# Performance work log

Measured on AMD Instinct MI355X. Metric: run time of the kernel, lower is better.

The kernel has to match this reference:

```python
import jax, jax.numpy as jnp
import numpy as np

N_NODES = 50000
N_EDGES = 600000
IN_DIM = 128
HIDDEN = 256
OUT_DIM = 16


def setup_inputs() -> dict:
    key = jax.random.key(0)
    ks = jax.random.split(key, 10)
    x = jax.random.normal(ks[0], (N_NODES, IN_DIM), dtype=jnp.float32)
    edge_index = jax.random.randint(ks[1], (2, N_EDGES), 0, N_NODES, dtype=jnp.int64)
    s = 0.05
    return {
        "x": x,
        "edge_index": edge_index,
        # conv1 MLP: Linear(IN_DIM->HIDDEN), Linear(HIDDEN->HIDDEN)
        "w1a": jax.random.normal(ks[2], (IN_DIM, HIDDEN), dtype=jnp.float32) * s,
        "b1a": jnp.zeros((HIDDEN,), dtype=jnp.float32),
        "w2a": jax.random.normal(ks[3], (HIDDEN, HIDDEN), dtype=jnp.float32) * s,
        "b2a": jnp.zeros((HIDDEN,), dtype=jnp.float32),
        # conv2 MLP: Linear(HIDDEN->HIDDEN), Linear(HIDDEN->OUT_DIM)
        "w1b": jax.random.normal(ks[4], (HIDDEN, HIDDEN), dtype=jnp.float32) * s,
        "b1b": jnp.zeros((HIDDEN,), dtype=jnp.float32),
        "w2b": jax.random.normal(ks[5], (HIDDEN, OUT_DIM), dtype=jnp.float32) * s,
        "b2b": jnp.zeros((OUT_DIM,), dtype=jnp.float32),
    }


def _gin_conv(h, src, dst, w1, b1, w2, b2):
    # GINConv with eps=0: MLP(h_i + sum_{j: (j->i)} h_j)
    agg = jax.ops.segment_sum(h[src], dst, num_segments=N_NODES)  # [N, D]
    z = h + agg
    z = jax.nn.relu(z @ w1 + b1)
    return z @ w2 + b2


def reference(x, edge_index, w1a, b1a, w2a, b2a, w1b, b1b, w2b, b2b):
    src, dst = edge_index[0], edge_index[1]
    h = _gin_conv(x, src, dst, w1a, b1a, w2a, b2a)
    h = jax.nn.relu(h)  # dropout p=0.0 -> identity
    h = _gin_conv(h, src, dst, w1b, b1b, w2b, b2b)
    return jax.nn.log_softmax(h, axis=1)
```

## Files before the change

### kernel.cpp

```cpp
#include <hip/hip_runtime.h>

#define NN 50000
#define NE 600000
#define SCAN_BLOCKS 196

typedef short v8s __attribute__((ext_vector_type(8)));
typedef float v4f __attribute__((ext_vector_type(4)));

#define LAW 72
#define MTW 264

__device__ __forceinline__ float b2f(ushort u) {
    union { unsigned u; float f; } v; v.u = ((unsigned)u) << 16; return v.f;
}
__device__ __forceinline__ float uaf(unsigned u) {
    union { unsigned u; float f; } v; v.u = u; return v.f;
}
__device__ __forceinline__ ushort f2b(float f) {
    union { float f; unsigned u; } v; v.f = f;
    unsigned r = v.u + 0x7FFFu + ((v.u >> 16) & 1u);
    return (ushort)(r >> 16);
}

__global__ __launch_bounds__(256) void detect_idx_kernel(const int* __restrict__ raw,
                                                          int* __restrict__ flag) {
    __shared__ int cnt;
    if (threadIdx.x == 0) cnt = 0;
    __syncthreads();
    int c = 0;
    for (int i = threadIdx.x; i < 2048; i += 256)
        if (raw[2 * i + 1] != 0) c++;
    atomicAdd(&cnt, c);
    __syncthreads();
    if (threadIdx.x == 0) *flag = (cnt > 10) ? 1 : 0;
}

__global__ __launch_bounds__(256) void convert_idx_kernel(const void* __restrict__ raw,
                                                           const int* __restrict__ flag,
                                                           int* __restrict__ out,
                                                           int* __restrict__ deg, int n) {
    int i = blockIdx.x * 256 + threadIdx.x;
    if (i >= n) return;
    int v;
    if (*flag) v = ((const int*)raw)[i];
    else       v = (int)((const long long*)raw)[i];
    out[i] = v;
    if (i >= NE) atomicAdd(&deg[v], 1);
}

__global__ __launch_bounds__(256) void block_sum_kernel(const int* __restrict__ deg,
                                                         int* __restrict__ bsum) {
    const int i = blockIdx.x * 256 + threadIdx.x;
    int v = (i < NN) ? deg[i] : 0;
#pragma unroll
    for (int o = 32; o; o >>= 1) v += __shfl_down(v, o, 64);
    __shared__ int ws[4];
    if ((threadIdx.x & 63) == 0) ws[threadIdx.x >> 6] = v;
    __syncthreads();
    if (threadIdx.x == 0) bsum[blockIdx.x] = ws[0] + ws[1] + ws[2] + ws[3];
}

__global__ __launch_bounds__(256) void scan_sums_kernel(const int* __restrict__ bsum,
                                                         int* __restrict__ boff,
                                                         int* __restrict__ rowptr) {
    __shared__ int tmp[256];
    const int t = threadIdx.x;
    const int v = (t < SCAN_BLOCKS) ? bsum[t] : 0;
    tmp[t] = v;
    __syncthreads();
#pragma unroll
    for (int off = 1; off < 256; off <<= 1) {
        int u = (t >= off) ? tmp[t - off] : 0;
        __syncthreads();
        tmp[t] += u;
        __syncthreads();
    }
    boff[t] = tmp[t] - v;
    if (t == 255) rowptr[NN] = tmp[255];
}

__global__ __launch_bounds__(256) void block_scan_kernel(const int* __restrict__ deg,
                                                          const int* __restrict__ boff,
                                                          int* __restrict__ rowptr,
                                                          int* __restrict__ cursor) {
    const int t = threadIdx.x;
    const int i = blockIdx.x * 256 + t;
    const int lane = t & 63, w = t >> 6;
    const int v = (i < NN) ? deg[i] : 0;
    int s = v;
#pragma unroll
    for (int o = 1; o < 64; o <<= 1) {
        int u = __shfl_up(s, o, 64);
        if (lane >= o) s += u;
    }
    __shared__ int wsum[4];
    if (lane == 63) wsum[w] = s;
    __syncthreads();
    int wpre = 0;
    for (int k = 0; k < w; k++) wpre += wsum[k];
    const int excl = boff[blockIdx.x] + wpre + s - v;
    if (i < NN) {
        rowptr[i] = excl;
        cursor[i] = excl;
    }
}

__global__ __launch_bounds__(256) void fill_csr_kernel(const int* __restrict__ srcIdx,
                                                        const int* __restrict__ dstIdx,
                                                        int* __restrict__ cursor,
                                                        int* __restrict__ csr_src) {
    int e = blockIdx.x * 256 + threadIdx.x;
    if (e >= NE) return;
    int pos = atomicAdd(&cursor[dstIdx[e]], 1);
    csr_src[pos] = srcIdx[e];
}

__global__ __launch_bounds__(256) void cvt_f32_bf16_kernel(const float* __restrict__ in,
                                                            ushort* __restrict__ out, int n4) {
    int i = blockIdx.x * 256 + threadIdx.x;
    if (i >= n4) return;
    const float4 v = *(const float4*)&in[(size_t)i * 4];
    ushort4 o;
    o.x = f2b(v.x); o.y = f2b(v.y); o.z = f2b(v.z); o.w = f2b(v.w);
    *(ushort4*)&out[(size_t)i * 4] = o;
}

__global__ __launch_bounds__(256) void pack_w1_kernel(const float* __restrict__ in,
                                                       ushort* __restrict__ out, int K1) {
    int o = blockIdx.x * 256 + threadIdx.x;
    if (o >= K1 * 256) return;
    int j = o & 7, lane = (o >> 3) & 63, f = o >> 9;
    int kk = f & 1, n = (f >> 1) & 3, wv = (f >> 3) & 3, s = f >> 5;
    int k = s * 64 + kk * 32 + (lane >> 4) * 8 + j;
    int col = wv * 64 + n * 16 + (lane & 15);
    out[o] = f2b(in[(size_t)k * 256 + col]);
}

__global__ __launch_bounds__(256) void pack_w2_kernel(const float* __restrict__ in,
                                                       ushort* __restrict__ out) {
    int o = blockIdx.x * 256 + threadIdx.x;
    if (o >= 256 * 256) return;
    int j = o & 7, lane = (o >> 3) & 63, f = o >> 9;
    int kk = f & 3, n = (f >> 2) & 3, wv = (f >> 4) & 3, kh = f >> 6;
    int k = kh * 128 + kk * 32 + (lane >> 4) * 8 + j;
    int col = wv * 64 + n * 16 + (lane & 15);
    out[o] = f2b(in[(size_t)k * 256 + col]);
}

__global__ __launch_bounds__(256) void pack_wh_kernel(const float* __restrict__ in,
                                                       ushort* __restrict__ out) {
    int o = blockIdx.x * 256 + threadIdx.x;
    if (o >= 4096) return;
    int j = o & 7, lane = (o >> 3) & 63, k8 = o >> 9;
    int k = k8 * 32 + (lane >> 4) * 8 + j;
    int col = lane & 15;
    out[o] = f2b(in[(size_t)k * 16 + col]);
}

template <int D>
__global__ __launch_bounds__(256) void aggregate_bf16_kernel(const ushort* __restrict__ feat,
                                                              ushort* __restrict__ z,
                                                              const int* __restrict__ rowptr,
                                                              const int* __restrict__ csr_src) {
    const int node = __builtin_amdgcn_readfirstlane(blockIdx.x * 4 + (threadIdx.x >> 6));
    const int lane = threadIdx.x & 63;
    if (node >= NN) return;
    const int rbeg = rowptr[node];
    const int rend = rowptr[node + 1];

    if constexpr (D == 256) {
        const size_t base = (size_t)node * 256 + lane * 4;
        const uint2 sv = *(const uint2*)&feat[base];
        float a0 = uaf(sv.x << 16), a1 = uaf(sv.x & 0xFFFF0000u);
        float a2 = uaf(sv.y << 16), a3 = uaf(sv.y & 0xFFFF0000u);
        int j = rbeg;
        for (; j + 7 < rend; j += 8) {
            uint2 v[8];
#pragma unroll
            for (int q = 0; q < 8; q++)
                v[q] = *(const uint2*)&feat[(size_t)csr_src[j + q] * 256 + lane * 4];
#pragma unroll
            for (int q = 0; q < 8; q++) {
                a0 += uaf(v[q].x << 16); a1 += uaf(v[q].x & 0xFFFF0000u);
                a2 += uaf(v[q].y << 16); a3 += uaf(v[q].y & 0xFFFF0000u);
            }
        }
        for (; j + 3 < rend; j += 4) {
            uint2 v[4];
#pragma unroll
            for (int q = 0; q < 4; q++)
                v[q] = *(const uint2*)&feat[(size_t)csr_src[j + q] * 256 + lane * 4];
#pragma unroll
            for (int q = 0; q < 4; q++) {
                a0 += uaf(v[q].x << 16); a1 += uaf(v[q].x & 0xFFFF0000u);
                a2 += uaf(v[q].y << 16); a3 += uaf(v[q].y & 0xFFFF0000u);
            }
        }
        for (; j < rend; j++) {
            const uint2 v = *(const uint2*)&feat[(size_t)csr_src[j] * 256 + lane * 4];
            a0 += uaf(v.x << 16); a1 += uaf(v.x & 0xFFFF0000u);
            a2 += uaf(v.y << 16); a3 += uaf(v.y & 0xFFFF0000u);
        }
        uint2 o;
        o.x = (uint)f2b(a0) | ((uint)f2b(a1) << 16);
        o.y = (uint)f2b(a2) | ((uint)f2b(a3) << 16);
        *(uint2*)&z[base] = o;
    } else {
        const size_t base = (size_t)node * 128 + lane * 2;
        const uint sv = *(const uint*)&feat[base];
        float a0 = uaf(sv << 16), a1 = uaf(sv & 0xFFFF0000u);
        int j = rbeg;
        for (; j + 7 < rend; j += 8) {
            uint v[8];
#pragma unroll
            for (int q = 0; q < 8; q++)
                v[q] = *(const uint*)&feat[(size_t)csr_src[j + q] * 128 + lane * 2];
#pragma unroll
            for (int q = 0; q < 8; q++) {
                a0 += uaf(v[q] << 16); a1 += uaf(v[q] & 0xFFFF0000u);
            }
        }
        for (; j + 3 < rend; j += 4) {
            uint v[4];
#pragma unroll
            for (int q = 0; q < 4; q++)
                v[q] = *(const uint*)&feat[(size_t)csr_src[j + q] * 128 + lane * 2];
#pragma unroll
            for (int q = 0; q < 4; q++) {
                a0 += uaf(v[q] << 16); a1 += uaf(v[q] & 0xFFFF0000u);
            }
        }
        for (; j < rend; j++) {
            const uint v = *(const uint*)&feat[(size_t)csr_src[j] * 128 + lane * 2];
            a0 += uaf(v << 16); a1 += uaf(v & 0xFFFF0000u);
        }
        *(uint*)&z[base] = (uint)f2b(a0) | ((uint)f2b(a1) << 16);
    }
}

template <int K1, bool HEAD>
__global__ __launch_bounds__(256) void fused_mlp_kernel(const ushort* __restrict__ A,
                                                         const ushort* __restrict__ W1p,
                                                         const float* __restrict__ b1,
                                                         const ushort* __restrict__ W2p,
                                                         const float* __restrict__ b2,
                                                         void* __restrict__ outp, int M) {
    constexpr int S = K1 / 64;
    __shared__ ushort lA[2][64 * LAW];
    __shared__ ushort mT[64 * MTW];
    const int tid = threadIdx.x;
    const int lane = tid & 63;
    const int wv = tid >> 6;
    const int row0 = blockIdx.x * 64;
    const int l15 = lane & 15;
    const int kq = lane >> 4;
    const int ar = tid >> 2, ak = (tid & 3) * 16;

    const bool aok = (row0 + ar) < M;
    const ushort* Arow = A + (size_t)(row0 + ar) * K1 + ak;

    v4f acc[4][4];
#pragma unroll
    for (int m = 0; m < 4; m++)
#pragma unroll
        for (int n = 0; n < 4; n++) acc[m][n] = (v4f){0.f, 0.f, 0.f, 0.f};

    v8s a0 = {}, a1v = {};
    v8s w1cur[4][2], w1nxt[4][2];

    if (aok) { a0 = *(const v8s*)Arow; a1v = *(const v8s*)(Arow + 8); }
#pragma unroll
    for (int n = 0; n < 4; n++)
#pragma unroll
        for (int kk = 0; kk < 2; kk++)
            w1cur[n][kk] = *(const v8s*)(W1p + (size_t)(wv * 8 + n * 2 + kk) * 512 + lane * 8);
    *(v8s*)&lA[0][ar * LAW + ak]     = a0;
    *(v8s*)&lA[0][ar * LAW + ak + 8] = a1v;

#pragma unroll
    for (int s = 0; s < S; s++) {
        __syncthreads();
        if (s + 1 < S) {
            a0 = (v8s){}; a1v = (v8s){};
            if (aok) {
                a0  = *(const v8s*)(Arow + (s + 1) * 64);
                a1v = *(const v8s*)(Arow + (s + 1) * 64 + 8);
            }
#pragma unroll
            for (int n = 0; n < 4; n++)
#pragma unroll
                for (int kk = 0; kk < 2; kk++)
                    w1nxt[n][kk] = *(const v8s*)(W1p + (size_t)((s + 1) * 32 + wv * 8 + n * 2 + kk) * 512 + lane * 8);
        }
        v8s af[4][2];
#pragma unroll
        for (int m = 0; m < 4; m++)
#pragma unroll
            for (int kk = 0; kk < 2; kk++)
                af[m][kk] = *(const v8s*)&lA[s & 1][(m * 16 + l15) * LAW + kk * 32 + kq * 8];
#pragma unroll
        for (int kk = 0; kk < 2; kk++)
#pragma unroll
            for (int m = 0; m < 4; m++)
#pragma unroll
                for (int n = 0; n < 4; n++)
                    acc[m][n] = __builtin_amdgcn_mfma_f32_16x16x32_bf16(af[m][kk], w1cur[n][kk], acc[m][n], 0, 0, 0);
        if (s + 1 < S) {
            *(v8s*)&lA[(s + 1) & 1][ar * LAW + ak]     = a0;
            *(v8s*)&lA[(s + 1) & 1][ar * LAW + ak + 8] = a1v;
#pragma unroll
            for (int n = 0; n < 4; n++)
#pragma unroll
                for (int kk = 0; kk < 2; kk++)
                    w1cur[n][kk] = w1nxt[n][kk];
        }
    }

#pragma unroll
    for (int n = 0; n < 4; n++) {
        const int gc = wv * 64 + n * 16 + l15;
        const float bv = b1[gc];
#pragma unroll
        for (int m = 0; m < 4; m++)
#pragma unroll
            for (int r = 0; r < 4; r++)
                mT[(m * 16 + kq * 4 + r) * MTW + gc] = f2b(fmaxf(acc[m][n][r] + bv, 0.f));
    }
    __syncthreads();

    if constexpr (!HEAD) {
#pragma unroll
        for (int m = 0; m < 4; m++)
#pragma unroll
            for (int n = 0; n < 4; n++) acc[m][n] = (v4f){0.f, 0.f, 0.f, 0.f};
#pragma unroll
        for (int kh = 0; kh < 2; kh++) {
            v8s w2r[4][4];
#pragma unroll
            for (int n = 0; n < 4; n++)
#pragma unroll
                for (int kk = 0; kk < 4; kk++)
                    w2r[n][kk] = *(const v8s*)(W2p + (size_t)(kh * 64 + wv * 16 + n * 4 + kk) * 512 + lane * 8);
#pragma unroll
            for (int kk = 0; kk < 4; kk++) {
                v8s a2[4];
#pragma unroll
                for (int m = 0; m < 4; m++)
                    a2[m] = *(const v8s*)&mT[(m * 16 + l15) * MTW + kh * 128 + kk * 32 + kq * 8];
#pragma unroll
                for (int m = 0; m < 4; m++)
#pragma unroll
                    for (int n = 0; n < 4; n++)
                        acc[m][n] = __builtin_amdgcn_mfma_f32_16x16x32_bf16(a2[m], w2r[n][kk], acc[m][n], 0, 0, 0);
            }
        }
        __syncthreads();
#pragma unroll
        for (int n = 0; n < 4; n++) {
            const int gc = wv * 64 + n * 16 + l15;
            const float bv = b2[gc];
#pragma unroll
            for (int m = 0; m < 4; m++)
#pragma unroll
                for (int r = 0; r < 4; r++)
                    mT[(m * 16 + kq * 4 + r) * MTW + gc] = f2b(fmaxf(acc[m][n][r] + bv, 0.f));
        }
        __syncthreads();
        ushort* C = (ushort*)outp;
        const int brow = tid >> 5, bcol = (tid & 31) * 8;
#pragma unroll
        for (int i = 0; i < 8; i++) {
            const int row = i * 8 + brow;
            if (row0 + row < M) {
                const v8s v = *(const v8s*)&mT[row * MTW + bcol];
                *(v8s*)&C[(size_t)(row0 + row) * 256 + bcol] = v;
            }
        }
    } else {
        v4f h = (v4f){0.f, 0.f, 0.f, 0.f};
        v8s w2r[8];
#pragma unroll
        for (int k8 = 0; k8 < 8; k8++)
            w2r[k8] = *(const v8s*)(W2p + (size_t)k8 * 512 + lane * 8);
#pragma unroll
        for (int k8 = 0; k8 < 8; k8++) {
            const v8s a2 = *(const v8s*)&mT[(wv * 16 + l15) * MTW + k8 * 32 + kq * 8];
            h = __builtin_amdgcn_mfma_f32_16x16x32_bf16(a2, w2r[k8], h, 0, 0, 0);
        }
        float* O = (float*)outp;
        const float bv = b2[l15];
#pragma unroll
        for (int r = 0; r < 4; r++) {
            const float v = h[r] + bv;
            float mx = v;
#pragma unroll
            for (int o = 8; o; o >>= 1) mx = fmaxf(mx, __shfl_xor(mx, o, 16));
            const float e = expf(v - mx);
            float sl = e;
#pragma unroll
            for (int o = 8; o; o >>= 1) sl += __shfl_xor(sl, o, 16);
            const int grow = row0 + wv * 16 + kq * 4 + r;
            if (grow < M) O[(size_t)grow * 16 + l15] = (v - mx) - logf(sl);
        }
    }
}

extern "C" void kernel_launch(void* const* d_in, const int* in_sizes, int n_in,
                              void* d_out, int out_size, void* d_ws, size_t ws_size,
                              hipStream_t stream) {
    (void)in_sizes; (void)n_in; (void)out_size; (void)ws_size;
    const float* x   = (const float*)d_in[0];
    const void*  ei  = d_in[1];
    const float* w1a = (const float*)d_in[2];
    const float* b1a = (const float*)d_in[3];
    const float* w2a = (const float*)d_in[4];
    const float* b2a = (const float*)d_in[5];
    const float* w1b = (const float*)d_in[6];
    const float* b1b = (const float*)d_in[7];
    const float* w2b = (const float*)d_in[8];
    const float* b2b = (const float*)d_in[9];
    float* out = (float*)d_out;

    ushort* XB   = (ushort*)d_ws;
    ushort* Z1   = XB + (size_t)NN * 128;
    ushort* H1   = Z1 + (size_t)NN * 128;
    ushort* Z2   = H1 + (size_t)NN * 256;
    ushort* W1pa = Z2 + (size_t)NN * 256;
    ushort* W2pa = W1pa + 128 * 256;
    ushort* W1pb = W2pa + 256 * 256;
    ushort* W2hp = W1pb + 256 * 256;
    int* idx     = (int*)(W2hp + 16 * 256);
    int* flag    = idx + 2 * NE;
    int* deg     = flag + 1;
    int* rowptr  = deg + NN;
    int* cursor  = rowptr + NN + 1;
    int* csr_src = cursor + NN;
    int* bsum    = csr_src + NE;
    int* boff    = bsum + SCAN_BLOCKS;

    detect_idx_kernel<<<1, 256, 0, stream>>>((const int*)ei, flag);
    hipMemsetAsync(deg, 0, NN * sizeof(int), stream);
    convert_idx_kernel<<<(2 * NE + 255) / 256, 256, 0, stream>>>(ei, flag, idx, deg, 2 * NE);
    const int* srcI = idx;
    const int* dstI = idx + NE;
    block_sum_kernel<<<SCAN_BLOCKS, 256, 0, stream>>>(deg, bsum);
    scan_sums_kernel<<<1, 256, 0, stream>>>(bsum, boff, rowptr);
    block_scan_kernel<<<SCAN_BLOCKS, 256, 0, stream>>>(deg, boff, rowptr, cursor);
    fill_csr_kernel<<<(NE + 255) / 256, 256, 0, stream>>>(srcI, dstI, cursor, csr_src);

    cvt_f32_bf16_kernel<<<(NN * 128 / 4 + 255) / 256, 256, 0, stream>>>(x, XB, NN * 128 / 4);
    pack_w1_kernel<<<(128 * 256 + 255) / 256, 256, 0, stream>>>(w1a, W1pa, 128);
    pack_w2_kernel<<<(256 * 256 + 255) / 256, 256, 0, stream>>>(w2a, W2pa);
    pack_w1_kernel<<<(256 * 256 + 255) / 256, 256, 0, stream>>>(w1b, W1pb, 256);
    pack_wh_kernel<<<(4096 + 255) / 256, 256, 0, stream>>>(w2b, W2hp);

    const int aggBlocks = (NN + 3) / 4;
    const int mlpBlocks = (NN + 63) / 64;

    aggregate_bf16_kernel<128><<<aggBlocks, 256, 0, stream>>>(XB, Z1, rowptr, csr_src);
    fused_mlp_kernel<128, false><<<mlpBlocks, 256, 0, stream>>>(Z1, W1pa, b1a, W2pa, b2a, H1, NN);

    aggregate_bf16_kernel<256><<<aggBlocks, 256, 0, stream>>>(H1, Z2, rowptr, csr_src);
    fused_mlp_kernel<256, true><<<mlpBlocks, 256, 0, stream>>>(Z2, W1pb, b1b, W2hp, b2b, out, NN);
}
```

Before: 201.8 us.

## Fuse neighbor aggregation into MLP kernel and read raw edge indices directly

The separate aggregation kernels are folded into the MLP kernel. Each block gathers and sums neighbor features for its 64 rows straight into shared memory, then runs the MFMA GEMMs from there, so the Z1/Z2 intermediates never round-trip through global memory. The edge-index conversion pass is dropped: degree counting and CSR fill read the raw int32 or int64 indices directly, and the four weight-packing launches are merged into one. In exchange the gather now runs at fewer waves per node block, with larger shared memory and no double-buffered A prefetch, which may lower occupancy and latency hiding during the gather.

```diff
diff --git a/kernel.cpp b/kernel.cpp
--- a/kernel.cpp
+++ b/kernel.cpp
@@ -7,12 +7,8 @@
 typedef short v8s __attribute__((ext_vector_type(8)));
 typedef float v4f __attribute__((ext_vector_type(4)));
 
-#define LAW 72
 #define MTW 264
 
-__device__ __forceinline__ float b2f(ushort u) {
-    union { unsigned u; float f; } v; v.u = ((unsigned)u) << 16; return v.f;
-}
 __device__ __forceinline__ float uaf(unsigned u) {
     union { unsigned u; float f; } v; v.u = u; return v.f;
 }
@@ -35,17 +31,15 @@
     if (threadIdx.x == 0) *flag = (cnt > 10) ? 1 : 0;
 }
 
-__global__ __launch_bounds__(256) void convert_idx_kernel(const void* __restrict__ raw,
-                                                           const int* __restrict__ flag,
-                                                           int* __restrict__ out,
-                                                           int* __restrict__ deg, int n) {
-    int i = blockIdx.x * 256 + threadIdx.x;
-    if (i >= n) return;
-    int v;
-    if (*flag) v = ((const int*)raw)[i];
-    else       v = (int)((const long long*)raw)[i];
-    out[i] = v;
-    if (i >= NE) atomicAdd(&deg[v], 1);
+__global__ __launch_bounds__(256) void count_deg_raw_kernel(const void* __restrict__ raw,
+                                                             const int* __restrict__ flag,
+                                                             int* __restrict__ deg) {
+    int e = blockIdx.x * 256 + threadIdx.x;
+    if (e >= NE) return;
+    int d;
+    if (*flag) d = ((const int*)raw)[NE + e];
+    else       d = (int)((const long long*)raw)[NE + e];
+    atomicAdd(&deg[d], 1);
 }
 
 __global__ __launch_bounds__(256) void block_sum_kernel(const int* __restrict__ deg,
@@ -105,14 +99,22 @@
     }
 }
 
-__global__ __launch_bounds__(256) void fill_csr_kernel(const int* __restrict__ srcIdx,
-                                                        const int* __restrict__ dstIdx,
-                                                        int* __restrict__ cursor,
-                                                        int* __restrict__ csr_src) {
+__global__ __launch_bounds__(256) void fill_csr_raw_kernel(const void* __restrict__ raw,
+                                                            const int* __restrict__ flag,
+                                                            int* __restrict__ cursor,
+                                                            int* __restrict__ csr_src) {
     int e = blockIdx.x * 256 + threadIdx.x;
     if (e >= NE) return;
-    int pos = atomicAdd(&cursor[dstIdx[e]], 1);
-    csr_src[pos] = srcIdx[e];
+    int s, d;
+    if (*flag) {
+        s = ((const int*)raw)[e];
+        d = ((const int*)raw)[NE + e];
+    } else {
+        s = (int)((const long long*)raw)[e];
+        d = (int)((const long long*)raw)[NE + e];
+    }
+    int pos = atomicAdd(&cursor[d], 1);
+    csr_src[pos] = s;
 }
 
 __global__ __launch_bounds__(256) void cvt_f32_bf16_kernel(const float* __restrict__ in,
@@ -125,128 +127,54 @@
     *(ushort4*)&out[(size_t)i * 4] = o;
 }
 
-__global__ __launch_bounds__(256) void pack_w1_kernel(const float* __restrict__ in,
-                                                       ushort* __restrict__ out, int K1) {
-    int o = blockIdx.x * 256 + threadIdx.x;
-    if (o >= K1 * 256) return;
+__device__ __forceinline__ void pack_w1_elem(const float* in, ushort* out, int o, int K1) {
     int j = o & 7, lane = (o >> 3) & 63, f = o >> 9;
     int kk = f & 1, n = (f >> 1) & 3, wv = (f >> 3) & 3, s = f >> 5;
     int k = s * 64 + kk * 32 + (lane >> 4) * 8 + j;
     int col = wv * 64 + n * 16 + (lane & 15);
     out[o] = f2b(in[(size_t)k * 256 + col]);
 }
-
-__global__ __launch_bounds__(256) void pack_w2_kernel(const float* __restrict__ in,
-                                                       ushort* __restrict__ out) {
-    int o = blockIdx.x * 256 + threadIdx.x;
-    if (o >= 256 * 256) return;
-    int j = o & 7, lane = (o >> 3) & 63, f = o >> 9;
-    int kk = f & 3, n = (f >> 2) & 3, wv = (f >> 4) & 3, kh = f >> 6;
-    int k = kh * 128 + kk * 32 + (lane >> 4) * 8 + j;
-    int col = wv * 64 + n * 16 + (lane & 15);
-    out[o] = f2b(in[(size_t)k * 256 + col]);
-}
-
-__global__ __launch_bounds__(256) void pack_wh_kernel(const float* __restrict__ in,
-                                                       ushort* __restrict__ out) {
-    int o = blockIdx.x * 256 + threadIdx.x;
-    if (o >= 4096) return;
-    int j = o & 7, lane = (o >> 3) & 63, k8 = o >> 9;
-    int k = k8 * 32 + (lane >> 4) * 8 + j;
-    int col = lane & 15;
-    out[o] = f2b(in[(size_t)k * 16 + col]);
-}
-
-template <int D>
-__global__ __launch_bounds__(256) void aggregate_bf16_kernel(const ushort* __restrict__ feat,
-                                                              ushort* __restrict__ z,
-                                                              const int* __restrict__ rowptr,
-                                                              const int* __restrict__ csr_src) {
-    const int node = __builtin_amdgcn_readfirstlane(blockIdx.x * 4 + (threadIdx.x >> 6));
-    const int lane = threadIdx.x & 63;
-    if (node >= NN) return;
-    const int rbeg = rowptr[node];
-    const int rend = rowptr[node + 1];
-
-    if constexpr (D == 256) {
-        const size_t base = (size_t)node * 256 + lane * 4;
-        const uint2 sv = *(const uint2*)&feat[base];
-        float a0 = uaf(sv.x << 16), a1 = uaf(sv.x & 0xFFFF0000u);
-        float a2 = uaf(sv.y << 16), a3 = uaf(sv.y & 0xFFFF0000u);
-        int j = rbeg;
-        for (; j + 7 < rend; j += 8) {
-            uint2 v[8];
-#pragma unroll
-            for (int q = 0; q < 8; q++)
-                v[q] = *(const uint2*)&feat[(size_t)csr_src[j + q] * 256 + lane * 4];
-#pragma unroll
-            for (int q = 0; q < 8; q++) {
-                a0 += uaf(v[q].x << 16); a1 += uaf(v[q].x & 0xFFFF0000u);
-                a2 += uaf(v[q].y << 16); a3 += uaf(v[q].y & 0xFFFF0000u);
-            }
-        }
-        for (; j + 3 < rend; j += 4) {
-            uint2 v[4];
-#pragma unroll
-            for (int q = 0; q < 4; q++)
-                v[q] = *(const uint2*)&feat[(size_t)csr_src[j + q] * 256 + lane * 4];
-#pragma unroll
-            for (int q = 0; q < 4; q++) {
-                a0 += uaf(v[q].x << 16); a1 += uaf(v[q].x & 0xFFFF0000u);
-                a2 += uaf(v[q].y << 16); a3 += uaf(v[q].y & 0xFFFF0000u);
-            }
-        }
-        for (; j < rend; j++) {
-            const uint2 v = *(const uint2*)&feat[(size_t)csr_src[j] * 256 + lane * 4];
-            a0 += uaf(v.x << 16); a1 += uaf(v.x & 0xFFFF0000u);
-            a2 += uaf(v.y << 16); a3 += uaf(v.y & 0xFFFF0000u);
-        }
-        uint2 o;
-        o.x = (uint)f2b(a0) | ((uint)f2b(a1) << 16);
-        o.y = (uint)f2b(a2) | ((uint)f2b(a3) << 16);
-        *(uint2*)&z[base] = o;
+__global__ __launch_bounds__(256) void pack_all_kernel(const float* __restrict__ w1a,
+                                                        const float* __restrict__ w2a,
+                                                        const float* __restrict__ w1b,
+                                                        const float* __restrict__ wh,
+                                                        ushort* __restrict__ W1pa,
+                                                        ushort* __restrict__ W2pa,
+                                                        ushort* __restrict__ W1pb,
+                                                        ushort* __restrict__ W2hp) {
+    const int b = blockIdx.x;
+    if (b < 128) {
+        pack_w1_elem(w1a, W1pa, b * 256 + threadIdx.x, 128);
+    } else if (b < 384) {
+        int o = (b - 128) * 256 + threadIdx.x;
+        int j = o & 7, lane = (o >> 3) & 63, f = o >> 9;
+        int kk = f & 3, n = (f >> 2) & 3, wv = (f >> 4) & 3, kh = f >> 6;
+        int k = kh * 128 + kk * 32 + (lane >> 4) * 8 + j;
+        int col = wv * 64 + n * 16 + (lane & 15);
+        W2pa[o] = f2b(w2a[(size_t)k * 256 + col]);
+    } else if (b < 640) {
+        pack_w1_elem(w1b, W1pb, (b - 384) * 256 + threadIdx.x, 256);
     } else {
-        const size_t base = (size_t)node * 128 + lane * 2;
-        const uint sv = *(const uint*)&feat[base];
-        float a0 = uaf(sv << 16), a1 = uaf(sv & 0xFFFF0000u);
-        int j = rbeg;
-        for (; j + 7 < rend; j += 8) {
-            uint v[8];
-#pragma unroll
-            for (int q = 0; q < 8; q++)
-                v[q] = *(const uint*)&feat[(size_t)csr_src[j + q] * 128 + lane * 2];
-#pragma unroll
-            for (int q = 0; q < 8; q++) {
-                a0 += uaf(v[q] << 16); a1 += uaf(v[q] & 0xFFFF0000u);
-            }
-        }
-        for (; j + 3 < rend; j += 4) {
-            uint v[4];
-#pragma unroll
-            for (int q = 0; q < 4; q++)
-                v[q] = *(const uint*)&feat[(size_t)csr_src[j + q] * 128 + lane * 2];
-#pragma unroll
-            for (int q = 0; q < 4; q++) {
-                a0 += uaf(v[q] << 16); a1 += uaf(v[q] & 0xFFFF0000u);
-            }
-        }
-        for (; j < rend; j++) {
-            const uint v = *(const uint*)&feat[(size_t)csr_src[j] * 128 + lane * 2];
-            a0 += uaf(v << 16); a1 += uaf(v & 0xFFFF0000u);
-        }
-        *(uint*)&z[base] = (uint)f2b(a0) | ((uint)f2b(a1) << 16);
+        int o = (b - 640) * 256 + threadIdx.x;
+        int j = o & 7, lane = (o >> 3) & 63, k8 = o >> 9;
+        int k = k8 * 32 + (lane >> 4) * 8 + j;
+        int col = lane & 15;
+        W2hp[o] = f2b(wh[(size_t)k * 16 + col]);
     }
 }
 
 template <int K1, bool HEAD>
-__global__ __launch_bounds__(256) void fused_mlp_kernel(const ushort* __restrict__ A,
+__global__ __launch_bounds__(256) void fused_gin_kernel(const ushort* __restrict__ feat,
+                                                         const int* __restrict__ rowptr,
+                                                         const int* __restrict__ csr_src,
                                                          const ushort* __restrict__ W1p,
                                                          const float* __restrict__ b1,
                                                          const ushort* __restrict__ W2p,
                                                          const float* __restrict__ b2,
                                                          void* __restrict__ outp, int M) {
     constexpr int S = K1 / 64;
-    __shared__ ushort lA[2][64 * LAW];
+    constexpr int ZW = K1 + 8;
+    __shared__ ushort zT[64 * ZW];
     __shared__ ushort mT[64 * MTW];
     const int tid = threadIdx.x;
     const int lane = tid & 63;
@@ -254,66 +182,113 @@
     const int row0 = blockIdx.x * 64;
     const int l15 = lane & 15;
     const int kq = lane >> 4;
-    const int ar = tid >> 2, ak = (tid & 3) * 16;
-
-    const bool aok = (row0 + ar) < M;
-    const ushort* Arow = A + (size_t)(row0 + ar) * K1 + ak;
+
+    for (int t = 0; t < 16; t++) {
+        const int r = wv * 16 + t;
+        const int node = __builtin_amdgcn_readfirstlane(row0 + r);
+        ushort* zrow = &zT[r * ZW];
+        if (node < M) {
+            const int rbeg = rowptr[node];
+            const int rend = rowptr[node + 1];
+            if constexpr (K1 == 256) {
+                const uint2 sv = *(const uint2*)&feat[(size_t)node * 256 + lane * 4];
+                float a0 = uaf(sv.x << 16), a1 = uaf(sv.x & 0xFFFF0000u);
+                float a2 = uaf(sv.y << 16), a3 = uaf(sv.y & 0xFFFF0000u);
+                int j = rbeg;
+                for (; j + 7 < rend; j += 8) {
+                    uint2 v[8];
+#pragma unroll
+                    for (int q = 0; q < 8; q++)
+                        v[q] = *(const uint2*)&feat[(size_t)csr_src[j + q] * 256 + lane * 4];
+#pragma unroll
+                    for (int q = 0; q < 8; q++) {
+                        a0 += uaf(v[q].x << 16); a1 += uaf(v[q].x & 0xFFFF0000u);
+                        a2 += uaf(v[q].y << 16); a3 += uaf(v[q].y & 0xFFFF0000u);
+                    }
+                }
+                for (; j + 3 < rend; j += 4) {
+                    uint2 v[4];
+#pragma unroll
+                    for (int q = 0; q < 4; q++)
+                        v[q] = *(const uint2*)&feat[(size_t)csr_src[j + q] * 256 + lane * 4];
+#pragma unroll
+                    for (int q = 0; q < 4; q++) {
+                        a0 += uaf(v[q].x << 16); a1 += uaf(v[q].x & 0xFFFF0000u);
+                        a2 += uaf(v[q].y << 16); a3 += uaf(v[q].y & 0xFFFF0000u);
+                    }
+                }
+                for (; j < rend; j++) {
+                    const uint2 v = *(const uint2*)&feat[(size_t)csr_src[j] * 256 + lane * 4];
+                    a0 += uaf(v.x << 16); a1 += uaf(v.x & 0xFFFF0000u);
+                    a2 += uaf(v.y << 16); a3 += uaf(v.y & 0xFFFF0000u);
+                }
+                uint2 o;
+                o.x = (uint)f2b(a0) | ((uint)f2b(a1) << 16);
+                o.y = (uint)f2b(a2) | ((uint)f2b(a3) << 16);
+                *(uint2*)&zrow[lane * 4] = o;
+            } else {
+                const uint sv = *(const uint*)&feat[(size_t)node * 128 + lane * 2];
+                float a0 = uaf(sv << 16), a1 = uaf(sv & 0xFFFF0000u);
+                int j = rbeg;
+                for (; j + 7 < rend; j += 8) {
+                    uint v[8];
+#pragma unroll
+                    for (int q = 0; q < 8; q++)
+                        v[q] = *(const uint*)&feat[(size_t)csr_src[j + q] * 128 + lane * 2];
+#pragma unroll
+                    for (int q = 0; q < 8; q++) {
+                        a0 += uaf(v[q] << 16); a1 += uaf(v[q] & 0xFFFF0000u);
+                    }
+                }
+                for (; j + 3 < rend; j += 4) {
+                    uint v[4];
+#pragma unroll
+                    for (int q = 0; q < 4; q++)
+                        v[q] = *(const uint*)&feat[(size_t)csr_src[j + q] * 128 + lane * 2];
+#pragma unroll
+                    for (int q = 0; q < 4; q++) {
+                        a0 += uaf(v[q] << 16); a1 += uaf(v[q] & 0xFFFF0000u);
+                    }
+                }
+                for (; j < rend; j++) {
+                    const uint v = *(const uint*)&feat[(size_t)csr_src[j] * 128 + lane * 2];
+                    a0 += uaf(v << 16); a1 += uaf(v & 0xFFFF0000u);
+                }
+                *(uint*)&zrow[lane * 2] = (uint)f2b(a0) | ((uint)f2b(a1) << 16);
+            }
+        } else {
+            if constexpr (K1 == 256) *(uint2*)&zrow[lane * 4] = (uint2){0u, 0u};
+            else                     *(uint*)&zrow[lane * 2] = 0u;
+        }
+    }
+    __syncthreads();
 
     v4f acc[4][4];
 #pragma unroll
     for (int m = 0; m < 4; m++)
 #pragma unroll
         for (int n = 0; n < 4; n++) acc[m][n] = (v4f){0.f, 0.f, 0.f, 0.f};
-
-    v8s a0 = {}, a1v = {};
-    v8s w1cur[4][2], w1nxt[4][2];
-
-    if (aok) { a0 = *(const v8s*)Arow; a1v = *(const v8s*)(Arow + 8); }
-#pragma unroll
-    for (int n = 0; n < 4; n++)
+#pragma unroll
+    for (int s = 0; s < S; s++) {
+        v8s w1r[4][2];
+#pragma unroll
+        for (int n = 0; n < 4; n++)
+#pragma unroll
+            for (int kk = 0; kk < 2; kk++)
+                w1r[n][kk] = *(const v8s*)(W1p + (size_t)(s * 32 + wv * 8 + n * 2 + kk) * 512 + lane * 8);
+        v8s af[4][2];
+#pragma unroll
+        for (int m = 0; m < 4; m++)
+#pragma unroll
+            for (int kk = 0; kk < 2; kk++)
+                af[m][kk] = *(const v8s*)&zT[(m * 16 + l15) * ZW + s * 64 + kk * 32 + kq * 8];
 #pragma unroll
         for (int kk = 0; kk < 2; kk++)
-            w1cur[n][kk] = *(const v8s*)(W1p + (size_t)(wv * 8 + n * 2 + kk) * 512 + lane * 8);
-    *(v8s*)&lA[0][ar * LAW + ak]     = a0;
-    *(v8s*)&lA[0][ar * LAW + ak + 8] = a1v;
-
-#pragma unroll
-    for (int s = 0; s < S; s++) {
-        __syncthreads();
-        if (s + 1 < S) {
-            a0 = (v8s){}; a1v = (v8s){};
-            if (aok) {
-                a0  = *(const v8s*)(Arow + (s + 1) * 64);
-                a1v = *(const v8s*)(Arow + (s + 1) * 64 + 8);
-            }
-#pragma unroll
-            for (int n = 0; n < 4; n++)
-#pragma unroll
-                for (int kk = 0; kk < 2; kk++)
-                    w1nxt[n][kk] = *(const v8s*)(W1p + (size_t)((s + 1) * 32 + wv * 8 + n * 2 + kk) * 512 + lane * 8);
-        }
-        v8s af[4][2];
-#pragma unroll
-        for (int m = 0; m < 4; m++)
-#pragma unroll
-            for (int kk = 0; kk < 2; kk++)
-                af[m][kk] = *(const v8s*)&lA[s & 1][(m * 16 + l15) * LAW + kk * 32 + kq * 8];
-#pragma unroll
-        for (int kk = 0; kk < 2; kk++)
 #pragma unroll
             for (int m = 0; m < 4; m++)
 #pragma unroll
                 for (int n = 0; n < 4; n++)
-                    acc[m][n] = __builtin_amdgcn_mfma_f32_16x16x32_bf16(af[m][kk], w1cur[n][kk], acc[m][n], 0, 0, 0);
-        if (s + 1 < S) {
-            *(v8s*)&lA[(s + 1) & 1][ar * LAW + ak]     = a0;
-            *(v8s*)&lA[(s + 1) & 1][ar * LAW + ak + 8] = a1v;
-#pragma unroll
-            for (int n = 0; n < 4; n++)
-#pragma unroll
-                for (int kk = 0; kk < 2; kk++)
-                    w1cur[n][kk] = w1nxt[n][kk];
-        }
+                    acc[m][n] = __builtin_amdgcn_mfma_f32_16x16x32_bf16(af[m][kk], w1r[n][kk], acc[m][n], 0, 0, 0);
     }
 
 #pragma unroll
@@ -422,15 +397,12 @@
     float* out = (float*)d_out;
 
     ushort* XB   = (ushort*)d_ws;
-    ushort* Z1   = XB + (size_t)NN * 128;
-    ushort* H1   = Z1 + (size_t)NN * 128;
-    ushort* Z2   = H1 + (size_t)NN * 256;
-    ushort* W1pa = Z2 + (size_t)NN * 256;
+    ushort* H1   = XB + (size_t)NN * 128;
+    ushort* W1pa = H1 + (size_t)NN * 256;
     ushort* W2pa = W1pa + 128 * 256;
     ushort* W1pb = W2pa + 256 * 256;
     ushort* W2hp = W1pb + 256 * 256;
-    int* idx     = (int*)(W2hp + 16 * 256);
-    int* flag    = idx + 2 * NE;
+    int* flag    = (int*)(W2hp + 16 * 256);
     int* deg     = flag + 1;
     int* rowptr  = deg + NN;
     int* cursor  = rowptr + NN + 1;
@@ -440,26 +412,20 @@
 
     detect_idx_kernel<<<1, 256, 0, stream>>>((const int*)ei, flag);
     hipMemsetAsync(deg, 0, NN * sizeof(int), stream);
-    convert_idx_kernel<<<(2 * NE + 255) / 256, 256, 0, stream>>>(ei, flag, idx, deg, 2 * NE);
-    const int* srcI = idx;
-    const int* dstI = idx + NE;
+    count_deg_raw_kernel<<<(NE + 255) / 256, 256, 0, stream>>>(ei, flag, deg);
     block_sum_kernel<<<SCAN_BLOCKS, 256, 0, stream>>>(deg, bsum);
     scan_sums_kernel<<<1, 256, 0, stream>>>(bsum, boff, rowptr);
     block_scan_kernel<<<SCAN_BLOCKS, 256, 0, stream>>>(deg, boff, rowptr, cursor);
-    fill_csr_kernel<<<(NE + 255) / 256, 256, 0, stream>>>(srcI, dstI, cursor, csr_src);
+    fill_csr_raw_kernel<<<(NE + 255) / 256, 256, 0, stream>>>(ei, flag, cursor, csr_src);
 
     cvt_f32_bf16_kernel<<<(NN * 128 / 4 + 255) / 256, 256, 0, stream>>>(x, XB, NN * 128 / 4);
-    pack_w1_kernel<<<(128 * 256 + 255) / 256, 256, 0, stream>>>(w1a, W1pa, 128);
-    pack_w2_kernel<<<(256 * 256 + 255) / 256, 256, 0, stream>>>(w2a, W2pa);
-    pack_w1_kernel<<<(256 * 256 + 255) / 256, 256, 0, stream>>>(w1b, W1pb, 256);
-    pack_wh_kernel<<<(4096 + 255) / 256, 256, 0, stream>>>(w2b, W2hp);
-
-    const int aggBlocks = (NN + 3) / 4;
-    const int mlpBlocks = (NN + 63) / 64;
-
-    aggregate_bf16_kernel<128><<<aggBlocks, 256, 0, stream>>>(XB, Z1, rowptr, csr_src);
-    fused_mlp_kernel<128, false><<<mlpBlocks, 256, 0, stream>>>(Z1, W1pa, b1a, W2pa, b2a, H1, NN);
-
-    aggregate_bf16_kernel<256><<<aggBlocks, 256, 0, stream>>>(H1, Z2, rowptr, csr_src);
-    fused_mlp_kernel<256, true><<<mlpBlocks, 256, 0, stream>>>(Z2, W1pb, b1b, W2hp, b2b, out, NN);
-}
+    pack_all_kernel<<<656, 256, 0, stream>>>(w1a, w2a, w1b, w2b, W1pa, W2pa, W1pb, W2hp);
+
+    const int ginBlocks = (NN + 63) / 64;
+
+    fused_gin_kernel<128, false><<<ginBlocks, 256, 0, stream>>>(
+        XB, rowptr, csr_src, W1pa, b1a, W2pa, b2a, H1, NN);
+
+    fused_gin_kernel<256, true><<<ginBlocks, 256, 0, stream>>>(
+        H1, rowptr, csr_src, W1pb, b1b, W2hp, b2b, out, NN);
+}
```

Measured after the change: 250.1 us. +23.9%, slower.
